# Kernel optimization log

Measured on AMD Instinct MI355X. Metric: run time of the kernel, lower is better.

Reference implementation:

```python
import jax, jax.numpy as jnp
import numpy as np

N, E = 10000, 160000
D, H, C, FF, L = 128, 4, 32, 512, 2
INNER = H * C
VOCAB, RELVOCAB = 32000, 100
EPS = 1e-6
GATE_BIAS = 3.0


def _layer_norm(x, w, b):
    mu = jnp.mean(x, axis=-1, keepdims=True)
    var = jnp.mean(jnp.square(x - mu), axis=-1, keepdims=True)
    return (x - mu) * jax.lax.rsqrt(var + EPS) * w + b


def setup_inputs() -> dict:
    key = jax.random.key(0)
    ks = jax.random.split(key, 24)
    s = 1.0 / np.sqrt(D)
    inp = {
        "node_ids": jax.random.randint(ks[0], (N,), 0, VOCAB),
        "edge_index": jax.random.randint(ks[1], (2, E), 0, N),
        "edge_ids": jax.random.randint(ks[2], (E,), 0, RELVOCAB),
        "node_emb": jax.random.normal(ks[3], (VOCAB, D), jnp.float32),
        "edge_emb": jax.random.normal(ks[4], (RELVOCAB, D), jnp.float32),
        # per-layer stacked params (torch Linear weight layout [out, in])
        "ln_w": jnp.ones((L, D), jnp.float32),
        "ln_b": jnp.zeros((L, D), jnp.float32),
        "q_w": jax.random.normal(ks[5], (L, INNER, D), jnp.float32) * (1.0 / np.sqrt(D * C)),
        "relA_w": jax.random.normal(ks[6], (L, FF, 2 * D), jnp.float32) * s,
        "relA_b": jnp.zeros((L, FF), jnp.float32),
        "relB_w": jax.random.normal(ks[7], (L, D, FF), jnp.float32) * s,
        "relB_b": jnp.zeros((L, D), jnp.float32),
        "relG_w": jax.random.normal(ks[8], (L, D, FF), jnp.float32) * s,
        "relG_b": jnp.zeros((L, D), jnp.float32),
        "k_w": jax.random.normal(ks[9], (L, INNER, 2 * D), jnp.float32) * s,
        "v_w": jax.random.normal(ks[10], (L, INNER, D), jnp.float32) * s,
        "o_w": jax.random.normal(ks[11], (L, D, INNER), jnp.float32) * (1.0 / np.sqrt(INNER)),
        "ff_ln_w": jnp.ones((L, D), jnp.float32),
        "ff_ln_b": jnp.zeros((L, D), jnp.float32),
        "wi_w": jax.random.normal(ks[12], (L, FF, D), jnp.float32) * s,
        "wo_w": jax.random.normal(ks[13], (L, D, FF), jnp.float32) * (1.0 / np.sqrt(FF)),
    }
    return inp


def _forward(node_ids, edge_index, edge_ids, node_emb, edge_emb, ln_w, ln_b,
             q_w, relA_w, relA_b, relB_w, relB_b, relG_w, relG_b,
             k_w, v_w, o_w, ff_ln_w, ff_ln_b, wi_w, wo_w):
    x = node_emb[node_ids]          # [N, D]
    ef = edge_emb[edge_ids]         # [E, D]
    src = edge_index[0]             # j (source / kv side)
    dst = edge_index[1]             # i (target / query side)
    for l in range(L):
        # --- relational self-attention ---
        q = _layer_norm(x, ln_w[l], ln_b[l])
        q = (q @ q_w[l].T).reshape(N, H, C)
        kv_j = x[src]                                   # [E, D]
        cat = jnp.concatenate([kv_j, ef], axis=-1)      # [E, 2D]
        inter = jax.nn.celu(cat @ relA_w[l].T + relA_b[l])   # [E, FF]
        gate = jax.nn.sigmoid(inter @ relG_w[l].T + relG_b[l] + GATE_BIAS)
        k_add = inter @ relB_w[l].T + relB_b[l]
        kv2 = kv_j * gate + k_add * (1.0 - gate)        # [E, D]
        k = (jnp.concatenate([kv2, ef], axis=-1) @ k_w[l].T).reshape(E, H, C)
        v = (kv2 @ v_w[l].T).reshape(E, H, C)
        scores = jnp.sum(q[dst] * k, axis=-1)           # [E, H]
        smax = jax.ops.segment_max(scores, dst, num_segments=N)
        ex = jnp.exp(scores - smax[dst])
        denom = jax.ops.segment_sum(ex, dst, num_segments=N)
        alpha = ex / denom[dst]                         # [E, H]
        msg = (v * alpha[..., None]).reshape(E, INNER)
        agg = jax.ops.segment_sum(msg, dst, num_segments=N)  # [N, INNER]
        x = x + agg @ o_w[l].T
        # --- feed-forward (T5-style, pre-LN, relu, residual) ---
        h = _layer_norm(x, ff_ln_w[l], ff_ln_b[l])
        x = x + jax.nn.relu(h @ wi_w[l].T) @ wo_w[l].T
    return x


def reference(node_ids, edge_index, edge_ids, node_emb, edge_emb, ln_w, ln_b,
              q_w, relA_w, relA_b, relB_w, relB_b, relG_w, relG_b,
              k_w, v_w, o_w, ff_ln_w, ff_ln_b, wi_w, wo_w):
    return _forward(node_ids, edge_index, edge_ids, node_emb, edge_emb, ln_w, ln_b,
                    q_w, relA_w, relA_b, relB_w, relB_b, relG_w, relG_b,
                    k_w, v_w, o_w, ff_ln_w, ff_ln_b, wi_w, wo_w)
```

## Files before the change

kernel.cpp:

```cpp
#include <hip/hip_runtime.h>
#include <hip/hip_bf16.h>

#define NN 10000
#define EE 160000
#define DD 128
#define HH 4
#define CC 32
#define FFF 512
#define LL 2
#define RELV 100
#define EPS 1e-6f
#define GATE_BIAS 3.0f
#define BM 64
#define NT 16

typedef __bf16 bf16x8 __attribute__((ext_vector_type(8)));
typedef float f32x4 __attribute__((ext_vector_type(4)));
typedef float f32x16 __attribute__((ext_vector_type(16)));

#define MFMA(a,b,c)   __builtin_amdgcn_mfma_f32_16x16x32_bf16((a),(b),(c),0,0,0)
#define MFMA32(a,b,c) __builtin_amdgcn_mfma_f32_32x32x16_bf16((a),(b),(c),0,0,0)

__device__ __forceinline__ int swzK(int e, int b){ return e*256 + (b ^ ((e&7)<<4)); }
__device__ __forceinline__ int swz128(int e, int b){ return e*256 + (b ^ ((e&7)<<4)); }
__device__ __forceinline__ int swz512(int e, int b){ return e*1024 + (b ^ ((e&7)<<4)); }

__device__ __forceinline__ void barrier_lgkm(){
  __builtin_amdgcn_sched_barrier(0);
  asm volatile("s_waitcnt lgkmcnt(0)" ::: "memory");
  __builtin_amdgcn_s_barrier();
  __builtin_amdgcn_sched_barrier(0);
}

__global__ __launch_bounds__(256) void k_gx(
    const int* __restrict__ node_ids, const float* __restrict__ node_emb,
    float* __restrict__ x, ushort* __restrict__ xb,
    const int* __restrict__ dst, int* __restrict__ hist){
  int b = blockIdx.x, t = threadIdx.x;
  int n = b*2 + (t>>7);
  int c = t & 127;
  float v = node_emb[(long)node_ids[n]*DD + c];
  x[(long)n*DD + c] = v;
  __hip_bfloat16 h = __float2bfloat16(v);
  xb[(long)n*DD + c] = *(ushort*)&h;
  if (t < 32){
    int e = b*32 + t;
    atomicAdd(&hist[dst[e]], 1);
  }
}

__device__ __forceinline__ void wprep_one(
    const float* __restrict__ in, ushort* __restrict__ out, int tid, int IN, int instride){
  int lane = tid & 63;
  int grp  = tid >> 6;
  int nkb  = IN >> 4;
  int kb   = grp % nkb;
  int cb   = grp / nkb;
  int col  = cb*32 + (lane & 31);
  int k0   = kb*16 + (lane >> 5)*8;
  const float* p = in + (long)col*instride + k0;
  bf16x8 h;
  #pragma unroll
  for (int j=0;j<8;++j) h[j] = (__bf16)p[j];
  *(bf16x8*)(out + (long)tid*8) = h;
}

__global__ __launch_bounds__(256) void k_prep(
    const float* __restrict__ relG_w, const float* __restrict__ relB_w,
    const float* __restrict__ k_w, const float* __restrict__ v_w,
    const float* __restrict__ relA_w,
    ushort* __restrict__ Gwb, ushort* __restrict__ Bwb,
    ushort* __restrict__ Kwb, ushort* __restrict__ Vwb, ushort* __restrict__ A1b){
  int tid = blockIdx.x*256 + threadIdx.x;
  if (tid < DD*FFF/8){
    wprep_one(relG_w, Gwb, tid, FFF, FFF);
    wprep_one(relB_w, Bwb, tid, FFF, FFF);
  }
  if (tid < DD*DD/8){
    wprep_one(k_w, Kwb, tid, DD, 256);
    wprep_one(v_w, Vwb, tid, DD, DD);
  }
  {
    int o = tid / DD, i = tid % DD;
    __hip_bfloat16 h = __float2bfloat16(relA_w[(long)o*256 + i]);
    A1b[tid] = *(ushort*)&h;
  }
}

__global__ __launch_bounds__(256) void k_f2b4(
    const float* __restrict__ q_w, const float* __restrict__ o_w,
    const float* __restrict__ wi_w, const float* __restrict__ wo_w,
    ushort* __restrict__ Qwb, ushort* __restrict__ Owb,
    ushort* __restrict__ Wib, ushort* __restrict__ Wob){
  long i = (long)blockIdx.x*256 + threadIdx.x;
  const long nV = (long)LL*DD*DD;
  if (i < nV){
    __hip_bfloat16 h1 = __float2bfloat16(q_w[i]); Qwb[i] = *(ushort*)&h1;
    __hip_bfloat16 h2 = __float2bfloat16(o_w[i]); Owb[i] = *(ushort*)&h2;
  }
  {
    __hip_bfloat16 h3 = __float2bfloat16(wi_w[i]); Wib[i] = *(ushort*)&h3;
    __hip_bfloat16 h4 = __float2bfloat16(wo_w[i]); Wob[i] = *(ushort*)&h4;
  }
}

__global__ __launch_bounds__(256) void k_ea(
    const float* __restrict__ edge_emb, const float* __restrict__ relA_w,
    const float* __restrict__ relA_b, const float* __restrict__ k_w,
    ushort* __restrict__ EA2b, float* __restrict__ EKf){
  int rel = blockIdx.x, t = threadIdx.x;
  __shared__ float emb[128];
  if (t < 128) emb[t] = edge_emb[(long)rel*DD + t];
  __syncthreads();
  for (int f=t; f<FFF; f+=256){
    const float* wr = relA_w + (long)f*256 + 128;
    float s = relA_b[f];
    for (int i=0;i<128;++i) s += emb[i]*wr[i];
    __hip_bfloat16 h = __float2bfloat16(s);
    EA2b[(long)rel*FFF + f] = *(ushort*)&h;
  }
  if (t < 128){
    const float* wr = k_w + (long)t*256 + 128;
    float s = 0.f;
    for (int i=0;i<128;++i) s += emb[i]*wr[i];
    EKf[(long)rel*DD + t] = s;
  }
}

__global__ __launch_bounds__(256) void k_scan(const int* __restrict__ hist, int* __restrict__ cursor){
  __shared__ int tsum[256];
  const int t = threadIdx.x;
  const int PER = (NN + 255) / 256;
  const int base = t*PER;
  int s = 0;
  for (int i=0;i<PER;++i){ int idx = base+i; if (idx < NN) s += hist[idx]; }
  tsum[t] = s;
  __syncthreads();
  if (t == 0){
    int run = 0;
    for (int i=0;i<256;++i){ int v = tsum[i]; tsum[i] = run; run += v; }
  }
  __syncthreads();
  int run = tsum[t];
  for (int i=0;i<PER;++i){
    int idx = base+i;
    if (idx < NN){ int v = hist[idx]; cursor[idx] = run; run += v; }
  }
}
__global__ __launch_bounds__(256) void k_scatter(const int* __restrict__ dst,
    int* __restrict__ cursor, int* __restrict__ perm){
  int e = blockIdx.x*256 + threadIdx.x;
  if (e < EE){
    int p = atomicAdd(&cursor[dst[e]], 1);
    perm[p] = e;
  }
}

__global__ __launch_bounds__(256) void k_lnq_xa(
    const float* __restrict__ x, const float* __restrict__ lnw, const float* __restrict__ lnb,
    const ushort* __restrict__ qwb, const ushort* __restrict__ a1b,
    float* __restrict__ q, ushort* __restrict__ XAb,
    float* __restrict__ agg, float* __restrict__ denom){
  __shared__ __align__(16) unsigned char HB[NT*256];
  __shared__ __align__(16) unsigned char HR[NT*256];
  const int n0 = blockIdx.x*NT;
  const int t = threadIdx.x;
  const int e = t>>4, s = t&15;
  const int w = t>>6, l = t&63, lr = l&15, lg = l>>4;
  {
    float4 z4 = {0.f,0.f,0.f,0.f};
    float* ap = agg + (long)n0*DD + t*8;
    *(float4*)ap = z4; *(float4*)(ap+4) = z4;
    if (t < NT*HH) denom[n0*HH + t] = 0.f;
  }
  {
    const float* xp = x + (long)(n0+e)*DD + s*8;
    float xv[8];
    *(float4*)&xv[0] = *(const float4*)xp;
    *(float4*)&xv[4] = *(const float4*)(xp+4);
    float sm = 0.f;
    #pragma unroll
    for (int i=0;i<8;++i) sm += xv[i];
    sm += __shfl_xor(sm,1); sm += __shfl_xor(sm,2);
    sm += __shfl_xor(sm,4); sm += __shfl_xor(sm,8);
    float mu = sm*(1.f/DD);
    float sq = 0.f;
    #pragma unroll
    for (int i=0;i<8;++i){ float d = xv[i]-mu; sq += d*d; }
    sq += __shfl_xor(sq,1); sq += __shfl_xor(sq,2);
    sq += __shfl_xor(sq,4); sq += __shfl_xor(sq,8);
    float rstd = rsqrtf(sq*(1.f/DD) + EPS);
    float4 w0 = *(const float4*)(lnw + s*8), w1 = *(const float4*)(lnw + s*8 + 4);
    float4 b0 = *(const float4*)(lnb + s*8), b1 = *(const float4*)(lnb + s*8 + 4);
    float wv[8] = {w0.x,w0.y,w0.z,w0.w,w1.x,w1.y,w1.z,w1.w};
    float bv[8] = {b0.x,b0.y,b0.z,b0.w,b1.x,b1.y,b1.z,b1.w};
    bf16x8 hb, hr;
    #pragma unroll
    for (int i=0;i<8;++i){
      hb[i] = (__bf16)((xv[i]-mu)*rstd*wv[i] + bv[i]);
      hr[i] = (__bf16)xv[i];
    }
    *(bf16x8*)(HB + swz128(e, s*16)) = hb;
    *(bf16x8*)(HR + swz128(e, s*16)) = hr;
  }
  __syncthreads();
  {
    const int o0 = w*32;
    f32x4 z = {0.f,0.f,0.f,0.f};
    f32x4 acc[2] = {z,z};
    #pragma unroll
    for (int k4=0;k4<4;++k4){
      bf16x8 a = *(const bf16x8*)(HB + swz128(lr, k4*64 + lg*16));
      #pragma unroll
      for (int nt=0;nt<2;++nt){
        bf16x8 b = *(const bf16x8*)(qwb + (long)(o0+nt*16+lr)*128 + k4*32 + lg*8);
        acc[nt] = MFMA(a, b, acc[nt]);
      }
    }
    #pragma unroll
    for (int nt=0;nt<2;++nt)
      #pragma unroll
      for (int r=0;r<4;++r)
        q[(long)(n0 + lg*4 + r)*DD + o0 + nt*16 + lr] = acc[nt][r];
  }
  {
    const int f0w = w*128;
    f32x4 z = {0.f,0.f,0.f,0.f};
    f32x4 acc[8] = {z,z,z,z,z,z,z,z};
    #pragma unroll
    for (int k4=0;k4<4;++k4){
      bf16x8 a = *(const bf16x8*)(HR + swz128(lr, k4*64 + lg*16));
      #pragma unroll
      for (int nt=0;nt<8;++nt){
        bf16x8 b = *(const bf16x8*)(a1b + (long)(f0w+nt*16+lr)*128 + k4*32 + lg*8);
        acc[nt] = MFMA(a, b, acc[nt]);
      }
    }
    #pragma unroll
    for (int nt=0;nt<8;++nt)
      #pragma unroll
      for (int r=0;r<4;++r){
        __hip_bfloat16 h = __float2bfloat16(acc[nt][r]);
        XAb[(long)(n0+lg*4+r)*FFF + f0w+nt*16+lr] = *(ushort*)&h;
      }
  }
}

__global__ __launch_bounds__(512,4) void k_edge(
    const ushort* __restrict__ xb, const ushort* __restrict__ XAb,
    const ushort* __restrict__ EAb, const float* __restrict__ EKf,
    const float* __restrict__ q,
    const int* __restrict__ src, const int* __restrict__ dst, const int* __restrict__ eids,
    const int* __restrict__ perm,
    const ushort* __restrict__ Gwb, const float* __restrict__ Gb,
    const ushort* __restrict__ Bwb, const float* __restrict__ Bb,
    const ushort* __restrict__ Kwb, const ushort* __restrict__ Vwb,
    float* __restrict__ agg, float* __restrict__ denom)
{
  __shared__ __align__(16) unsigned char KVB[BM*256];
  __shared__ __align__(16) unsigned char INTB[2][BM*256];
  __shared__ float EXL[BM][HH];
  __shared__ int srcl[BM], dstl[BM], eidl[BM];

  const int e0 = blockIdx.x * BM;
  const int t  = threadIdx.x;
  const int w  = t >> 6;
  const int l  = t & 63;
  const int c32 = l & 31;
  const int hi  = l >> 5;
  const int R = w >> 2;
  const int C = w & 3;
  const int oc = C*32 + c32;

  if (t < BM){
    int pe = perm[e0+t];
    srcl[t] = src[pe]; dstl[t] = dst[pe]; eidl[t] = eids[pe];
  }
  barrier_lgkm();

  {
    const uint4* xbu = (const uint4*)xb;
    #pragma unroll
    for (int it=0; it<2; ++it){
      int g = it*512 + t;
      int e = g >> 4, qq = g & 15;
      *(uint4*)(KVB + swzK(e, qq*16)) = xbu[(long)srcl[e]*16 + qq];
    }
  }

  f32x16 gbG, gbB;
  {
    float bg = Gb[oc] + GATE_BIAS;
    float bb = Bb[oc];
    #pragma unroll
    for (int i=0;i<16;++i){ gbG[i] = bg; gbB[i] = bb; }
  }

  bf16x8 xa8[2], ea8[2];
  #pragma unroll
  for (int it=0; it<2; ++it){
    int g = it*512 + t;
    int e = g >> 4, c8 = g & 15;
    xa8[it] = *(const bf16x8*)(XAb + (long)srcl[e]*FFF + c8*8);
    ea8[it] = *(const bf16x8*)(EAb + (long)eidl[e]*FFF + c8*8);
  }

  #pragma unroll
  for (int ch=0; ch<4; ++ch){
    bf16x8 o[2];
    #pragma unroll
    for (int it=0; it<2; ++it){
      #pragma unroll
      for (int j=0;j<8;++j){
        float s = (float)xa8[it][j] + (float)ea8[it][j];
        o[it][j] = (__bf16)((s > 0.f) ? s : (__expf(s) - 1.f));
      }
    }
    unsigned char* INTp = INTB[ch & 1];
    #pragma unroll
    for (int it=0; it<2; ++it){
      int g = it*512 + t;
      int e = g >> 4, c8 = g & 15;
      *(bf16x8*)(INTp + swzK(e, c8*16)) = o[it];
    }
    barrier_lgkm();
    if (ch < 3){
      #pragma unroll
      for (int it=0; it<2; ++it){
        int g = it*512 + t;
        int e = g >> 4, c8 = g & 15;
        xa8[it] = *(const bf16x8*)(XAb + (long)srcl[e]*FFF + (ch+1)*128 + c8*8);
        ea8[it] = *(const bf16x8*)(EAb + (long)eidl[e]*FFF + (ch+1)*128 + c8*8);
      }
    }
    {
      const ushort* Wg = Gwb + ((long)(C*32 + ch*8)*64 + l)*8;
      bf16x8 wf[8];
      #pragma unroll
      for (int i=0;i<8;++i) wf[i] = *(const bf16x8*)(Wg + (long)i*512);
      #pragma unroll
      for (int i=0;i<8;++i){
        bf16x8 a = *(const bf16x8*)(INTp + swzK(R*32 + c32, i*32 + hi*16));
        gbG = MFMA32(a, wf[i], gbG);
      }
    }
    {
      const ushort* Wb = Bwb + ((long)(C*32 + ch*8)*64 + l)*8;
      bf16x8 wf[8];
      #pragma unroll
      for (int i=0;i<8;++i) wf[i] = *(const bf16x8*)(Wb + (long)i*512);
      #pragma unroll
      for (int i=0;i<8;++i){
        bf16x8 a = *(const bf16x8*)(INTp + swzK(R*32 + c32, i*32 + hi*16));
        gbB = MFMA32(a, wf[i], gbB);
      }
    }
  }

  #pragma unroll
  for (int r=0;r<16;++r){
    int row = (r&3) + 8*(r>>2) + 4*hi;
    int gr = R*32 + row;
    float g  = 1.f/(1.f + __expf(-gbG[r]));
    float kv = (float)*(const __bf16*)(KVB + swzK(gr, oc*2));
    float k2 = gbB[r] + g*(kv - gbB[r]);
    *(__bf16*)(KVB + swzK(gr, oc*2)) = (__bf16)k2;
  }
  barrier_lgkm();

  f32x16 ka, va;
  #pragma unroll
  for (int i=0;i<16;++i){ ka[i] = 0.f; va[i] = 0.f; }
  {
    const ushort* Wk = Kwb + ((long)(C*8)*64 + l)*8;
    bf16x8 wf[8];
    #pragma unroll
    for (int i=0;i<8;++i) wf[i] = *(const bf16x8*)(Wk + (long)i*512);
    #pragma unroll
    for (int i=0;i<8;++i){
      bf16x8 a = *(const bf16x8*)(KVB + swzK(R*32 + c32, i*32 + hi*16));
      ka = MFMA32(a, wf[i], ka);
    }
  }
  {
    const ushort* Wv = Vwb + ((long)(C*8)*64 + l)*8;
    bf16x8 wf[8];
    #pragma unroll
    for (int i=0;i<8;++i) wf[i] = *(const bf16x8*)(Wv + (long)i*512);
    #pragma unroll
    for (int i=0;i<8;++i){
      bf16x8 a = *(const bf16x8*)(KVB + swzK(R*32 + c32, i*32 + hi*16));
      va = MFMA32(a, wf[i], va);
    }
  }
  barrier_lgkm();

  #pragma unroll
  for (int r=0;r<16;++r){
    int row = (r&3) + 8*(r>>2) + 4*hi;
    int gr = R*32 + row;
    unsigned char* ab = (gr < 32) ? KVB : INTB[0];
    *(float*)(ab + ((gr & 31)*128 + oc)*4) = va[r];
  }
  #pragma unroll
  for (int r=0;r<16;++r){
    int row = (r&3) + 8*(r>>2) + 4*hi;
    int gr = R*32 + row;
    int dn = dstl[gr];
    float kv = ka[r] + EKf[(long)eidl[gr]*DD + oc];
    float p = kv * q[(long)dn*DD + oc];
    p += __shfl_xor(p, 1); p += __shfl_xor(p, 2);
    p += __shfl_xor(p, 4); p += __shfl_xor(p, 8);
    p += __shfl_xor(p, 16);
    if (c32 == 0) EXL[gr][C] = __expf(p);
  }
  barrier_lgkm();

  {
    const int col = t & 127;
    const int rg  = t >> 7;
    const int r0  = rg*16;
    const int h   = col >> 5;
    const unsigned char* ab = (rg < 2) ? KVB : INTB[0];
    const int rb = (rg & 1) * 16;
    float acc = 0.f;
    int cur = dstl[r0];
    for (int r=0; r<16; ++r){
      int dn = dstl[r0+r];
      if (dn != cur){
        atomicAdd(&agg[(long)cur*DD + col], acc);
        acc = 0.f; cur = dn;
      }
      acc += *(const float*)(ab + ((rb + r)*128 + col)*4) * EXL[r0+r][h];
    }
    atomicAdd(&agg[(long)cur*DD + col], acc);
    if (col < HH){
      float da = 0.f; int cur2 = dstl[r0];
      for (int r=r0; r<r0+16; ++r){
        int dn = dstl[r];
        if (dn != cur2){
          atomicAdd(&denom[cur2*HH + col], da);
          da = 0.f; cur2 = dn;
        }
        da += EXL[r][col];
      }
      atomicAdd(&denom[cur2*HH + col], da);
    }
  }
}

__global__ __launch_bounds__(256) void k_node(
    const float* __restrict__ agg, const float* __restrict__ denom,
    const ushort* __restrict__ owb,
    const float* __restrict__ lnw, const float* __restrict__ lnb,
    const ushort* __restrict__ wib, const ushort* __restrict__ wob,
    float* __restrict__ x, ushort* __restrict__ xb){
  __shared__ __align__(16) unsigned char AB[NT*256];
  __shared__ __align__(16) unsigned char IB[NT*1024];
  __shared__ __align__(16) float XO[NT][132];
  const int n0 = blockIdx.x*NT;
  const int t = threadIdx.x;
  const int e = t>>4, s = t&15;
  const int w = t>>6, l = t&63, lr = l&15, lg = l>>4;

  {
    const float* ap = agg + (long)(n0+e)*DD + s*8;
    float av[8];
    *(float4*)&av[0] = *(const float4*)ap;
    *(float4*)&av[4] = *(const float4*)(ap+4);
    float dinv = 1.f / denom[(n0+e)*HH + (s>>2)];
    bf16x8 hb;
    #pragma unroll
    for (int i=0;i<8;++i) hb[i] = (__bf16)(av[i]*dinv);
    *(bf16x8*)(AB + swz128(e, s*16)) = hb;
  }
  __syncthreads();

  {
    const int o0 = w*32;
    f32x4 z = {0.f,0.f,0.f,0.f};
    f32x4 acc[2] = {z,z};
    #pragma unroll
    for (int k4=0;k4<4;++k4){
      bf16x8 a = *(const bf16x8*)(AB + swz128(lr, k4*64 + lg*16));
      #pragma unroll
      for (int nt=0;nt<2;++nt){
        bf16x8 b = *(const bf16x8*)(owb + (long)(o0+nt*16+lr)*128 + k4*32 + lg*8);
        acc[nt] = MFMA(a, b, acc[nt]);
      }
    }
    #pragma unroll
    for (int nt=0;nt<2;++nt)
      #pragma unroll
      for (int r=0;r<4;++r)
        XO[lg*4+r][o0+nt*16+lr] = acc[nt][r];
  }
  __syncthreads();

  float x1[8];
  {
    const float* xp = x + (long)(n0+e)*DD + s*8;
    float xv[8];
    *(float4*)&xv[0] = *(const float4*)xp;
    *(float4*)&xv[4] = *(const float4*)(xp+4);
    #pragma unroll
    for (int i=0;i<8;++i) x1[i] = xv[i] + XO[e][s*8+i];
    float sm = 0.f;
    #pragma unroll
    for (int i=0;i<8;++i) sm += x1[i];
    sm += __shfl_xor(sm,1); sm += __shfl_xor(sm,2);
    sm += __shfl_xor(sm,4); sm += __shfl_xor(sm,8);
    float mu = sm*(1.f/DD);
    float sq = 0.f;
    #pragma unroll
    for (int i=0;i<8;++i){ float d = x1[i]-mu; sq += d*d; }
    sq += __shfl_xor(sq,1); sq += __shfl_xor(sq,2);
    sq += __shfl_xor(sq,4); sq += __shfl_xor(sq,8);
    float rstd = rsqrtf(sq*(1.f/DD) + EPS);
    float4 w0 = *(const float4*)(lnw + s*8), w1 = *(const float4*)(lnw + s*8 + 4);
    float4 b0 = *(const float4*)(lnb + s*8), b1 = *(const float4*)(lnb + s*8 + 4);
    float wv[8] = {w0.x,w0.y,w0.z,w0.w,w1.x,w1.y,w1.z,w1.w};
    float bv[8] = {b0.x,b0.y,b0.z,b0.w,b1.x,b1.y,b1.z,b1.w};
    bf16x8 hb;
    #pragma unroll
    for (int i=0;i<8;++i) hb[i] = (__bf16)((x1[i]-mu)*rstd*wv[i] + bv[i]);
    __syncthreads();
    *(bf16x8*)(AB + swz128(e, s*16)) = hb;
  }
  __syncthreads();

  {
    const int f0w = w*128;
    f32x4 z = {0.f,0.f,0.f,0.f};
    f32x4 acc[8] = {z,z,z,z,z,z,z,z};
    #pragma unroll
    for (int k4=0;k4<4;++k4){
      bf16x8 a = *(const bf16x8*)(AB + swz128(lr, k4*64 + lg*16));
      #pragma unroll
      for (int nt=0;nt<8;++nt){
        bf16x8 b = *(const bf16x8*)(wib + (long)(f0w+nt*16+lr)*128 + k4*32 + lg*8);
        acc[nt] = MFMA(a, b, acc[nt]);
      }
    }
    #pragma unroll
    for (int nt=0;nt<8;++nt)
      #pragma unroll
      for (int r=0;r<4;++r){
        int e2 = lg*4 + r;
        int f = f0w + nt*16 + lr;
        float va = acc[nt][r];
        *(__bf16*)(IB + swz512(e2, f*2)) = (__bf16)fmaxf(va, 0.f);
      }
  }
  __syncthreads();

  {
    const int o0 = w*32;
    f32x4 z = {0.f,0.f,0.f,0.f};
    f32x4 acc[2] = {z,z};
    #pragma unroll
    for (int k16=0;k16<16;++k16){
      bf16x8 a = *(const bf16x8*)(IB + swz512(lr, k16*64 + lg*16));
      #pragma unroll
      for (int nt=0;nt<2;++nt){
        bf16x8 b = *(const bf16x8*)(wob + (long)(o0+nt*16+lr)*512 + k16*32 + lg*8);
        acc[nt] = MFMA(a, b, acc[nt]);
      }
    }
    #pragma unroll
    for (int nt=0;nt<2;++nt)
      #pragma unroll
      for (int r=0;r<4;++r)
        XO[lg*4+r][o0+nt*16+lr] = acc[nt][r];
  }
  __syncthreads();

  {
    float xn[8];
    #pragma unroll
    for (int i=0;i<8;++i) xn[i] = x1[i] + XO[e][s*8+i];
    float* xp = x + (long)(n0+e)*DD + s*8;
    *(float4*)xp = *(float4*)&xn[0];
    *(float4*)(xp+4) = *(float4*)&xn[4];
    bf16x8 hb;
    #pragma unroll
    for (int i=0;i<8;++i) hb[i] = (__bf16)xn[i];
    *(bf16x8*)(xb + (long)(n0+e)*DD + s*8) = hb;
  }
}

extern "C" void kernel_launch(void* const* d_in, const int* in_sizes, int n_in,
                              void* d_out, int out_size, void* d_ws, size_t ws_size,
                              hipStream_t stream) {
  const int* node_ids   = (const int*)d_in[0];
  const int* edge_index = (const int*)d_in[1];
  const int* edge_ids   = (const int*)d_in[2];
  const float* node_emb = (const float*)d_in[3];
  const float* edge_emb = (const float*)d_in[4];
  const float* ln_w   = (const float*)d_in[5];
  const float* ln_b   = (const float*)d_in[6];
  const float* q_w    = (const float*)d_in[7];
  const float* relA_w = (const float*)d_in[8];
  const float* relA_b = (const float*)d_in[9];
  const float* relB_w = (const float*)d_in[10];
  const float* relB_b = (const float*)d_in[11];
  const float* relG_w = (const float*)d_in[12];
  const float* relG_b = (const float*)d_in[13];
  const float* k_w    = (const float*)d_in[14];
  const float* v_w    = (const float*)d_in[15];
  const float* o_w    = (const float*)d_in[16];
  const float* ff_ln_w= (const float*)d_in[17];
  const float* ff_ln_b= (const float*)d_in[18];
  const float* wi_w   = (const float*)d_in[19];
  const float* wo_w   = (const float*)d_in[20];
  const int* src = edge_index;
  const int* dst = edge_index + EE;

  float* ws = (float*)d_ws;
  float* x   = ws;  ws += (long)NN*DD;
  float* q   = ws;  ws += (long)NN*DD;
  float* denom = ws; ws += NN*HH;
  float* agg   = ws; ws += (long)NN*DD;
  float* EKf   = ws; ws += (long)LL*RELV*DD;
  int* hist   = (int*)ws; ws += NN;
  int* perm   = (int*)ws; ws += EE;
  ushort* xb  = (ushort*)ws; ws += (long)NN*DD/2;
  ushort* XAb = (ushort*)ws; ws += (long)NN*FFF/2;
  ushort* EAb = (ushort*)ws; ws += (long)LL*RELV*FFF/2;
  ushort* A1b = (ushort*)ws; ws += (long)LL*FFF*DD/2;
  ushort* Gwb = (ushort*)ws; ws += (long)LL*DD*FFF/2;
  ushort* Bwb = (ushort*)ws; ws += (long)LL*DD*FFF/2;
  ushort* Kwb = (ushort*)ws; ws += (long)LL*DD*DD/2;
  ushort* Vwb = (ushort*)ws; ws += (long)LL*DD*DD/2;
  ushort* Qwb = (ushort*)ws; ws += (long)LL*DD*DD/2;
  ushort* Owb = (ushort*)ws; ws += (long)LL*DD*DD/2;
  ushort* Wib = (ushort*)ws; ws += (long)LL*FFF*DD/2;
  ushort* Wob = (ushort*)ws; ws += (long)LL*DD*FFF/2;

  hipMemsetAsync(hist, 0, NN*sizeof(int), stream);
  k_gx<<<NN/2, 256, 0, stream>>>(node_ids, node_emb, x, xb, dst, hist);
  k_scan<<<1, 256, 0, stream>>>(hist, hist);
  k_scatter<<<(EE+255)/256, 256, 0, stream>>>(dst, hist, perm);
  for (int l=0; l<LL; ++l){
    k_prep<<<256, 256, 0, stream>>>(
        relG_w + (long)l*DD*FFF, relB_w + (long)l*DD*FFF,
        k_w + (long)l*DD*256,    v_w + (long)l*DD*DD,
        relA_w + (long)l*FFF*256,
        Gwb + (long)l*DD*FFF, Bwb + (long)l*DD*FFF,
        Kwb + (long)l*DD*DD,  Vwb + (long)l*DD*DD, A1b + (long)l*FFF*DD);
    k_ea<<<RELV, 256, 0, stream>>>(edge_emb, relA_w + (long)l*FFF*256, relA_b + (long)l*FFF,
                                   k_w + (long)l*DD*256, EAb + (long)l*RELV*FFF, EKf + (long)l*RELV*DD);
  }
  k_f2b4<<<512, 256, 0, stream>>>(q_w, o_w, wi_w, wo_w, Qwb, Owb, Wib, Wob);

  for (int l=0; l<LL; ++l){
    k_lnq_xa<<<NN/NT, 256, 0, stream>>>(x, ln_w + l*DD, ln_b + l*DD,
        Qwb + (long)l*DD*DD, A1b + (long)l*FFF*DD, q, XAb, agg, denom);
    k_edge<<<EE/BM, 512, 0, stream>>>(xb, XAb, EAb + (long)l*RELV*FFF, EKf + (long)l*RELV*DD,
        q, src, dst, edge_ids, perm,
        Gwb + (long)l*DD*FFF,  relG_b + (long)l*DD,
        Bwb + (long)l*DD*FFF,  relB_b + (long)l*DD,
        Kwb + (long)l*DD*DD,   Vwb + (long)l*DD*DD,
        agg, denom);
    k_node<<<NN/NT, 256, 0, stream>>>(agg, denom, Owb + (long)l*DD*DD,
        ff_ln_w + l*DD, ff_ln_b + l*DD,
        Wib + (long)l*FFF*DD, Wob + (long)l*DD*FFF, x, xb);
  }
  hipMemcpyAsync(d_out, x, (size_t)NN*DD*sizeof(float), hipMemcpyDeviceToDevice, stream);
}
```

Measured before the change: 454.0 us.

## Fuse next-layer LN+Q/XA projection into k_node and remap edge blocks per XCD

The next layer's layer norm, Q projection and XA projection, plus zeroing of agg/denom, now run at the end of k_node for the first layer. This removes one kernel launch and a re-read of x. k_edge blocks are remapped so that consecutive edge tiles land on the same XCD, which should improve L2 locality for the dst-sorted atomics. The custom lgkm barrier is replaced with plain __syncthreads. Zeroing agg inside k_node is safe only because each block zeroes its own rows after reading them.

```diff
diff --git a/kernel.cpp b/kernel.cpp
--- a/kernel.cpp
+++ b/kernel.cpp
@@ -24,13 +24,6 @@
 __device__ __forceinline__ int swzK(int e, int b){ return e*256 + (b ^ ((e&7)<<4)); }
 __device__ __forceinline__ int swz128(int e, int b){ return e*256 + (b ^ ((e&7)<<4)); }
 __device__ __forceinline__ int swz512(int e, int b){ return e*1024 + (b ^ ((e&7)<<4)); }
-
-__device__ __forceinline__ void barrier_lgkm(){
-  __builtin_amdgcn_sched_barrier(0);
-  asm volatile("s_waitcnt lgkmcnt(0)" ::: "memory");
-  __builtin_amdgcn_s_barrier();
-  __builtin_amdgcn_sched_barrier(0);
-}
 
 __global__ __launch_bounds__(256) void k_gx(
     const int* __restrict__ node_ids, const float* __restrict__ node_emb,
@@ -262,7 +255,15 @@
   __shared__ float EXL[BM][HH];
   __shared__ int srcl[BM], dstl[BM], eidl[BM];
 
-  const int e0 = blockIdx.x * BM;
+  int nb;
+  {
+    const int nwg = EE/BM;
+    const int q0 = nwg >> 3;
+    const int r0 = nwg & 7;
+    int xcd = blockIdx.x & 7, sub = blockIdx.x >> 3;
+    nb = (xcd < r0 ? xcd*(q0+1) : r0*(q0+1) + (xcd - r0)*q0) + sub;
+  }
+  const int e0 = nb * BM;
   const int t  = threadIdx.x;
   const int w  = t >> 6;
   const int l  = t & 63;
@@ -276,7 +277,7 @@
     int pe = perm[e0+t];
     srcl[t] = src[pe]; dstl[t] = dst[pe]; eidl[t] = eids[pe];
   }
-  barrier_lgkm();
+  __syncthreads();
 
   {
     const uint4* xbu = (const uint4*)xb;
@@ -323,7 +324,7 @@
       int e = g >> 4, c8 = g & 15;
       *(bf16x8*)(INTp + swzK(e, c8*16)) = o[it];
     }
-    barrier_lgkm();
+    __syncthreads();
     if (ch < 3){
       #pragma unroll
       for (int it=0; it<2; ++it){
@@ -366,7 +367,7 @@
     float k2 = gbB[r] + g*(kv - gbB[r]);
     *(__bf16*)(KVB + swzK(gr, oc*2)) = (__bf16)k2;
   }
-  barrier_lgkm();
+  __syncthreads();
 
   f32x16 ka, va;
   #pragma unroll
@@ -393,7 +394,7 @@
       va = MFMA32(a, wf[i], va);
     }
   }
-  barrier_lgkm();
+  __syncthreads();
 
   #pragma unroll
   for (int r=0;r<16;++r){
@@ -414,7 +415,7 @@
     p += __shfl_xor(p, 16);
     if (c32 == 0) EXL[gr][C] = __expf(p);
   }
-  barrier_lgkm();
+  __syncthreads();
 
   {
     const int col = t & 127;
@@ -449,12 +450,16 @@
   }
 }
 
+template<bool FUSE_LNQ>
 __global__ __launch_bounds__(256) void k_node(
     const float* __restrict__ agg, const float* __restrict__ denom,
     const ushort* __restrict__ owb,
     const float* __restrict__ lnw, const float* __restrict__ lnb,
     const ushort* __restrict__ wib, const ushort* __restrict__ wob,
-    float* __restrict__ x, ushort* __restrict__ xb){
+    float* __restrict__ x, ushort* __restrict__ xb,
+    const float* __restrict__ nlnw, const float* __restrict__ nlnb,
+    const ushort* __restrict__ nqwb, const ushort* __restrict__ na1b,
+    float* __restrict__ q, ushort* __restrict__ XAb){
   __shared__ __align__(16) unsigned char AB[NT*256];
   __shared__ __align__(16) unsigned char IB[NT*1024];
   __shared__ __align__(16) float XO[NT][132];
@@ -575,8 +580,8 @@
   }
   __syncthreads();
 
-  {
-    float xn[8];
+  float xn[8];
+  {
     #pragma unroll
     for (int i=0;i<8;++i) xn[i] = x1[i] + XO[e][s*8+i];
     float* xp = x + (long)(n0+e)*DD + s*8;
@@ -586,6 +591,82 @@
     #pragma unroll
     for (int i=0;i<8;++i) hb[i] = (__bf16)xn[i];
     *(bf16x8*)(xb + (long)(n0+e)*DD + s*8) = hb;
+  }
+
+  if constexpr (FUSE_LNQ){
+    {
+      float4 z4 = {0.f,0.f,0.f,0.f};
+      float* ap = (float*)agg + (long)n0*DD + t*8;
+      *(float4*)ap = z4; *(float4*)(ap+4) = z4;
+      if (t < NT*HH) ((float*)denom)[n0*HH + t] = 0.f;
+    }
+    {
+      float sm = 0.f;
+      #pragma unroll
+      for (int i=0;i<8;++i) sm += xn[i];
+      sm += __shfl_xor(sm,1); sm += __shfl_xor(sm,2);
+      sm += __shfl_xor(sm,4); sm += __shfl_xor(sm,8);
+      float mu = sm*(1.f/DD);
+      float sq = 0.f;
+      #pragma unroll
+      for (int i=0;i<8;++i){ float d = xn[i]-mu; sq += d*d; }
+      sq += __shfl_xor(sq,1); sq += __shfl_xor(sq,2);
+      sq += __shfl_xor(sq,4); sq += __shfl_xor(sq,8);
+      float rstd = rsqrtf(sq*(1.f/DD) + EPS);
+      float4 w0 = *(const float4*)(nlnw + s*8), w1 = *(const float4*)(nlnw + s*8 + 4);
+      float4 b0 = *(const float4*)(nlnb + s*8), b1 = *(const float4*)(nlnb + s*8 + 4);
+      float wv[8] = {w0.x,w0.y,w0.z,w0.w,w1.x,w1.y,w1.z,w1.w};
+      float bv[8] = {b0.x,b0.y,b0.z,b0.w,b1.x,b1.y,b1.z,b1.w};
+      bf16x8 hb, hr;
+      #pragma unroll
+      for (int i=0;i<8;++i){
+        hb[i] = (__bf16)((xn[i]-mu)*rstd*wv[i] + bv[i]);
+        hr[i] = (__bf16)xn[i];
+      }
+      *(bf16x8*)(AB + swz128(e, s*16)) = hb;
+      *(bf16x8*)(IB + swz128(e, s*16)) = hr;
+    }
+    __syncthreads();
+    {
+      const int o0 = w*32;
+      f32x4 z = {0.f,0.f,0.f,0.f};
+      f32x4 acc[2] = {z,z};
+      #pragma unroll
+      for (int k4=0;k4<4;++k4){
+        bf16x8 a = *(const bf16x8*)(AB + swz128(lr, k4*64 + lg*16));
+        #pragma unroll
+        for (int nt=0;nt<2;++nt){
+          bf16x8 b = *(const bf16x8*)(nqwb + (long)(o0+nt*16+lr)*128 + k4*32 + lg*8);
+          acc[nt] = MFMA(a, b, acc[nt]);
+        }
+      }
+      #pragma unroll
+      for (int nt=0;nt<2;++nt)
+        #pragma unroll
+        for (int r=0;r<4;++r)
+          q[(long)(n0 + lg*4 + r)*DD + o0 + nt*16 + lr] = acc[nt][r];
+    }
+    {
+      const int f0w = w*128;
+      f32x4 z = {0.f,0.f,0.f,0.f};
+      f32x4 acc[8] = {z,z,z,z,z,z,z,z};
+      #pragma unroll
+      for (int k4=0;k4<4;++k4){
+        bf16x8 a = *(const bf16x8*)(IB + swz128(lr, k4*64 + lg*16));
+        #pragma unroll
+        for (int nt=0;nt<8;++nt){
+          bf16x8 b = *(const bf16x8*)(na1b + (long)(f0w+nt*16+lr)*128 + k4*32 + lg*8);
+          acc[nt] = MFMA(a, b, acc[nt]);
+        }
+      }
+      #pragma unroll
+      for (int nt=0;nt<8;++nt)
+        #pragma unroll
+        for (int r=0;r<4;++r){
+          __hip_bfloat16 h = __float2bfloat16(acc[nt][r]);
+          XAb[(long)(n0+lg*4+r)*FFF + f0w+nt*16+lr] = *(ushort*)&h;
+        }
+    }
   }
 }
 
@@ -653,18 +734,26 @@
   }
   k_f2b4<<<512, 256, 0, stream>>>(q_w, o_w, wi_w, wo_w, Qwb, Owb, Wib, Wob);
 
+  k_lnq_xa<<<NN/NT, 256, 0, stream>>>(x, ln_w, ln_b, Qwb, A1b, q, XAb, agg, denom);
   for (int l=0; l<LL; ++l){
-    k_lnq_xa<<<NN/NT, 256, 0, stream>>>(x, ln_w + l*DD, ln_b + l*DD,
-        Qwb + (long)l*DD*DD, A1b + (long)l*FFF*DD, q, XAb, agg, denom);
     k_edge<<<EE/BM, 512, 0, stream>>>(xb, XAb, EAb + (long)l*RELV*FFF, EKf + (long)l*RELV*DD,
         q, src, dst, edge_ids, perm,
         Gwb + (long)l*DD*FFF,  relG_b + (long)l*DD,
         Bwb + (long)l*DD*FFF,  relB_b + (long)l*DD,
         Kwb + (long)l*DD*DD,   Vwb + (long)l*DD*DD,
         agg, denom);
-    k_node<<<NN/NT, 256, 0, stream>>>(agg, denom, Owb + (long)l*DD*DD,
-        ff_ln_w + l*DD, ff_ln_b + l*DD,
-        Wib + (long)l*FFF*DD, Wob + (long)l*DD*FFF, x, xb);
+    if (l < LL-1){
+      k_node<true><<<NN/NT, 256, 0, stream>>>(agg, denom, Owb + (long)l*DD*DD,
+          ff_ln_w + l*DD, ff_ln_b + l*DD,
+          Wib + (long)l*FFF*DD, Wob + (long)l*DD*FFF, x, xb,
+          ln_w + (l+1)*DD, ln_b + (l+1)*DD,
+          Qwb + (long)(l+1)*DD*DD, A1b + (long)(l+1)*FFF*DD, q, XAb);
+    } else {
+      k_node<false><<<NN/NT, 256, 0, stream>>>(agg, denom, Owb + (long)l*DD*DD,
+          ff_ln_w + l*DD, ff_ln_b + l*DD,
+          Wib + (long)l*FFF*DD, Wob + (long)l*DD*FFF, x, xb,
+          nullptr, nullptr, nullptr, nullptr, nullptr, nullptr);
+    }
   }
   hipMemcpyAsync(d_out, x, (size_t)NN*DD*sizeof(float), hipMemcpyDeviceToDevice, stream);
 }
```

Result: faster. 438.7 us (-3.4%).
